# Kernel tuning notes

Hardware: AMD Instinct MI355X
Metric: run time of the kernel (lower is better)

## Reference

```python
import jax, jax.numpy as jnp
import numpy as np

B, C, H, W = 16, 128, 64, 64
L, ND = 512, 256
GROUPS = 32
EPS = 1e-6


def setup_inputs() -> dict:
    key = jax.random.key(0)
    ks = jax.random.split(key, 8)
    return {
        "x": jax.random.normal(ks[0], (B, C, H, W), dtype=jnp.float32),
        "nd": jax.random.normal(ks[1], (B, L, ND), dtype=jnp.float32),
        "gn_gamma": jnp.ones((C,), dtype=jnp.float32),
        "gn_beta": jnp.zeros((C,), dtype=jnp.float32),
        "q_w": jax.random.normal(ks[2], (C, C), dtype=jnp.float32) * 0.02,
        "q_b": jax.random.normal(ks[3], (C,), dtype=jnp.float32) * 0.02,
        "nd_w": jax.random.normal(ks[4], (C, ND), dtype=jnp.float32) * 0.02,
        "nd_b": jax.random.normal(ks[5], (C,), dtype=jnp.float32) * 0.02,
        "proj_w": jax.random.normal(ks[6], (C, C), dtype=jnp.float32) * 0.02,
        "proj_b": jax.random.normal(ks[7], (C,), dtype=jnp.float32) * 0.02,
    }


def _group_norm(x, gamma, beta):
    b, c, h, w = x.shape
    xr = x.reshape(b, GROUPS, c // GROUPS, h, w)
    mean = xr.mean(axis=(2, 3, 4), keepdims=True)
    var = xr.var(axis=(2, 3, 4), keepdims=True)
    xn = ((xr - mean) * jax.lax.rsqrt(var + EPS)).reshape(b, c, h, w)
    return xn * gamma[None, :, None, None] + beta[None, :, None, None]


def reference(x, nd, gn_gamma, gn_beta, q_w, q_b, nd_w, nd_b, proj_w, proj_b):
    b, c, h, w = x.shape
    hn = _group_norm(x, gn_gamma, gn_beta)
    # 1x1 conv query -> [b, hw, c]
    q = jnp.einsum('bchw,oc->bhwo', hn, q_w).reshape(b, h * w, c) + q_b
    # silu + linear projection of conditioning; k and v use identical projection/input
    kv = jax.nn.silu(nd) @ nd_w.T + nd_b  # [b, L, c]
    # attention: [b, hw, L]
    logits = jnp.einsum('bnc,blc->bnl', q, kv) * (c ** -0.5)
    attn = jax.nn.softmax(logits, axis=2)
    # weighted sum of v -> [b, c, hw] -> [b, c, h, w]
    out = jnp.einsum('blc,bnl->bcn', kv, attn).reshape(b, c, h, w)
    # 1x1 conv projection
    out = jnp.einsum('bchw,oc->bohw', out, proj_w) + proj_b[None, :, None, None]
    return x + out
```

## Files before the change

kernel.cpp:

```cpp
#include <hip/hip_runtime.h>
#include <math.h>

constexpr int kB = 16, kC = 128, kHW = 4096, kL = 512, kND = 256, kG = 32;
constexpr float kEps = 1e-6f;
constexpr float kScale = 0.08838834764831845f;

typedef short sv8 __attribute__((ext_vector_type(8)));
typedef int   iv4 __attribute__((ext_vector_type(4)));
typedef float f32x16 __attribute__((ext_vector_type(16)));

static __device__ __forceinline__ unsigned short f2bf(float f) {
    unsigned int u = __builtin_bit_cast(unsigned int, f);
    u += 0x7fffu + ((u >> 16) & 1u);
    return (unsigned short)(u >> 16);
}
static __device__ __forceinline__ float bf2f(unsigned short s) {
    unsigned int u = ((unsigned int)s) << 16;
    return __builtin_bit_cast(float, u);
}
static __device__ __forceinline__ unsigned int pack2(float a, float b) {
    return (unsigned int)f2bf(a) | ((unsigned int)f2bf(b) << 16);
}

#define GLOAD_LDS16(gp, lp)                                                     \
    __builtin_amdgcn_global_load_lds(                                           \
        (const __attribute__((address_space(1))) void*)(gp),                    \
        (__attribute__((address_space(3))) void*)(lp), 16, 0, 0)

__global__ __launch_bounds__(256) void prep_all_k(
    const float* __restrict__ x, const float* __restrict__ nd,
    const float* __restrict__ nd_w, const float* __restrict__ nd_b,
    const float* __restrict__ proj_w, const float* __restrict__ q_w,
    float* __restrict__ stats, unsigned short* __restrict__ kv_bf,
    unsigned short* __restrict__ kvT_bf, unsigned short* __restrict__ pwb,
    unsigned short* __restrict__ qwb)
{
    __shared__ float s_lds[8][256];
    __shared__ float w_lds[128][68];
    __shared__ float t_lds[8][129];
    __shared__ float red8[8];
    const int bid = blockIdx.x;
    const int tid = threadIdx.x;

    if (bid < 512) {
        const float4* p4 = (const float4*)(x + (size_t)bid * 4 * kHW);
        float s = 0.f, ss = 0.f;
        for (int i = tid; i < 4096; i += 256) {
            float4 v = p4[i];
            s  += (v.x + v.y) + (v.z + v.w);
            ss += (v.x * v.x + v.y * v.y) + (v.z * v.z + v.w * v.w);
        }
#pragma unroll
        for (int off = 1; off < 64; off <<= 1) {
            s  += __shfl_xor(s, off, 64);
            ss += __shfl_xor(ss, off, 64);
        }
        int wid = tid >> 6;
        if ((tid & 63) == 0) { red8[wid] = s; red8[wid + 4] = ss; }
        __syncthreads();
        if (tid == 0) {
            float S  = (red8[0] + red8[1]) + (red8[2] + red8[3]);
            float SS = (red8[4] + red8[5]) + (red8[6] + red8[7]);
            float mean = S * (1.f / 16384.f);
            float var  = SS * (1.f / 16384.f) - mean * mean;
            stats[bid * 2]     = mean;
            stats[bid * 2 + 1] = rsqrtf(var + kEps);
        }
        return;
    }
    if (bid >= 1536) {
        const float* src = (bid < 1552) ? proj_w : q_w;
        unsigned short* dst = (bid < 1552) ? pwb : qwb;
        int i = (((bid - 1536) & 15) * 256 + tid) * 4;
        float4 v = *(const float4*)(src + i);
        dst[i + 0] = f2bf(v.x); dst[i + 1] = f2bf(v.y);
        dst[i + 2] = f2bf(v.z); dst[i + 3] = f2bf(v.w);
        return;
    }
    {
        int idx0 = bid - 512;
        int b = idx0 >> 6;
        int l0 = (idx0 & 63) * 8;
        const float4* ndp = (const float4*)(nd + ((size_t)b * kL + l0) * kND);
#pragma unroll
        for (int r = 0; r < 2; r++) {
            int idx = tid + r * 256;
            int row = idx >> 6;
            int c4 = idx & 63;
            float4 v = ndp[row * 64 + c4];
            v.x = v.x / (1.f + __expf(-v.x));
            v.y = v.y / (1.f + __expf(-v.y));
            v.z = v.z / (1.f + __expf(-v.z));
            v.w = v.w / (1.f + __expf(-v.w));
            *(float4*)&s_lds[row][c4 * 4] = v;
        }
        float acc[4] = {0.f, 0.f, 0.f, 0.f};
        int lr = tid >> 5;
        int oq = tid & 31;
        for (int d0 = 0; d0 < kND; d0 += 64) {
            __syncthreads();
#pragma unroll
            for (int r = 0; r < 8; r++) {
                int idx = tid + r * 256;
                int row = idx >> 4;
                int c4 = idx & 15;
                float4 v = ((const float4*)(nd_w + (size_t)row * kND + d0))[c4];
                *(float4*)&w_lds[row][c4 * 4] = v;
            }
            __syncthreads();
            for (int dd = 0; dd < 64; dd += 4) {
                float4 sv = *(const float4*)&s_lds[lr][d0 + dd];
#pragma unroll
                for (int j = 0; j < 4; j++) {
                    float4 wv = *(const float4*)&w_lds[oq + 32 * j][dd];
                    acc[j] += sv.x * wv.x + sv.y * wv.y + sv.z * wv.z + sv.w * wv.w;
                }
            }
        }
#pragma unroll
        for (int j = 0; j < 4; j++) {
            int o = oq + 32 * j;
            float vout = acc[j] + nd_b[o];
            kv_bf[((size_t)b * kL + l0 + lr) * kC + o] = f2bf(vout);
            t_lds[lr][o] = vout;
        }
        __syncthreads();
        int o = tid >> 1, lh = (tid & 1) * 4;
        unsigned long long pk = 0;
#pragma unroll
        for (int i = 0; i < 4; i++)
            pk |= (unsigned long long)f2bf(t_lds[lh + i][o]) << (16 * i);
        *(unsigned long long*)(kvT_bf + ((size_t)b * kC + o) * kL + l0 + lh) = pk;
    }
}

__global__ __launch_bounds__(128, 2) void attn_k(
    const float* __restrict__ x,
    const float* __restrict__ stats,
    const float* __restrict__ gamma,
    const float* __restrict__ beta,
    const unsigned short* __restrict__ qwb,
    const float* __restrict__ q_b,
    const unsigned short* __restrict__ kvb,
    const unsigned short* __restrict__ kvtb,
    const unsigned short* __restrict__ pwb,
    const float* __restrict__ proj_b,
    float* __restrict__ out)
{
    __shared__ __align__(16) char smem[33024];

    const int flat = blockIdx.y * gridDim.x + blockIdx.x;
    const int b  = ((flat & 7) << 1) | ((flat >> 3) & 1);
    const int n0 = (flat >> 4) * 64;
    const int tid = threadIdx.x;
    const int wave = tid >> 6;
    const int lane = tid & 63;
    const int lrow = lane & 31;
    const int hi = lane >> 5;
    const int swzA = (lrow & 15) << 4;
    const int swzT = ((lrow >> 1) & 3) << 4;

    const unsigned short* kvB  = kvb  + (size_t)b * kL * kC;
    const unsigned short* kvtB = kvtb + (size_t)b * kC * kL;

#define STAGE_TILE(tt) do {                                                     \
        int l0s = (tt) << 5;                                                    \
        char* dA = smem + (((tt) & 1) * 8192);                                  \
        char* dT = smem + 16384 + (((tt) & 1) * 8192);                          \
        _Pragma("unroll")                                                       \
        for (int i = 0; i < 4; i++) {                                           \
            int idx = i * 128 + wave * 64 + lane;                               \
            int l = idx >> 4, ch = idx & 15;                                    \
            const unsigned short* gs =                                          \
                kvB + (size_t)(l0s + l) * kC + ((ch ^ (l & 15)) * 8);           \
            GLOAD_LDS16(gs, dA + (i * 128 + wave * 64) * 16);                   \
        }                                                                       \
        _Pragma("unroll")                                                       \
        for (int i = 0; i < 4; i++) {                                           \
            int idx = i * 128 + wave * 64 + lane;                               \
            int c = idx >> 2, ch = idx & 3;                                     \
            const unsigned short* gs =                                          \
                kvtB + (size_t)c * kL + l0s + ((ch ^ ((c >> 1) & 3)) * 8);      \
            GLOAD_LDS16(gs, dT + (i * 128 + wave * 64) * 16);                   \
        }                                                                       \
    } while (0)

    STAGE_TILE(0);

    float* hn_f = (float*)(smem + 8192);
    f32x16 dq[4];
#pragma unroll
    for (int ot = 0; ot < 4; ot++)
#pragma unroll
        for (int r = 0; r < 16; r++) dq[ot][r] = 0.f;

    for (int cc = 0; cc < 4; cc++) {
#pragma unroll
        for (int k = 0; k < 4; k++) {
            int cl = k * 8 + (tid >> 4);
            int c = cc * 32 + cl;
            int n4 = tid & 15;
            float4 v = *(const float4*)(
                x + ((size_t)b * kC + c) * kHW + n0 + n4 * 4);
            float mean = stats[(b * kG + (c >> 2)) * 2];
            float rstd = stats[(b * kG + (c >> 2)) * 2 + 1];
            float ga = gamma[c] * rstd;
            float be = beta[c] - mean * ga;
            v.x = v.x * ga + be; v.y = v.y * ga + be;
            v.z = v.z * ga + be; v.w = v.w * ga + be;
            *(float4*)&hn_f[cl * 64 + n4 * 4] = v;
        }
        __syncthreads();
        sv8 bh[2];
#pragma unroll
        for (int kk = 0; kk < 2; kk++) {
            sv8 a;
#pragma unroll
            for (int j = 0; j < 8; j++)
                a[j] = (short)f2bf(hn_f[(kk * 16 + hi * 8 + j) * 64 + wave * 32 + lrow]);
            bh[kk] = a;
        }
#pragma unroll
        for (int ot = 0; ot < 4; ot++) {
            const unsigned short* arow =
                qwb + (size_t)(ot * 32 + lrow) * kC + cc * 32 + hi * 8;
#pragma unroll
            for (int kk = 0; kk < 2; kk++)
                dq[ot] = __builtin_amdgcn_mfma_f32_32x32x16_bf16(
                             *(const sv8*)(arow + kk * 16), bh[kk], dq[ot], 0, 0, 0);
        }
        __syncthreads();
    }
    sv8 qa[8];
#pragma unroll
    for (int ot = 0; ot < 4; ot++) {
        unsigned int pk[4], pk2[4];
#pragma unroll
        for (int g = 0; g < 4; g++) {
            int ob = ot * 32 + 8 * g + 4 * hi;
            float4 qb4 = *(const float4*)(q_b + ob);
            float v0 = (dq[ot][4 * g + 0] + qb4.x) * kScale;
            float v1 = (dq[ot][4 * g + 1] + qb4.y) * kScale;
            float v2 = (dq[ot][4 * g + 2] + qb4.z) * kScale;
            float v3 = (dq[ot][4 * g + 3] + qb4.w) * kScale;
            pk[g]  = pack2(v0, v1);
            pk2[g] = pack2(v2, v3);
        }
#pragma unroll
        for (int kk = 0; kk < 2; kk++) {
            unsigned int a_lo = pk[kk * 2],  a_hi = pk[kk * 2 + 1];
            unsigned int b_lo = pk2[kk * 2], b_hi = pk2[kk * 2 + 1];
            unsigned int own_a = hi ? a_hi : a_lo;
            unsigned int own_b = hi ? b_hi : b_lo;
            unsigned int rcv_a = (unsigned int)__shfl_xor((int)(hi ? a_lo : a_hi), 32, 64);
            unsigned int rcv_b = (unsigned int)__shfl_xor((int)(hi ? b_lo : b_hi), 32, 64);
            iv4 w;
            w[0] = (int)(hi ? rcv_a : own_a);
            w[1] = (int)(hi ? rcv_b : own_b);
            w[2] = (int)(hi ? own_a : rcv_a);
            w[3] = (int)(hi ? own_b : rcv_b);
            qa[2 * ot + kk] = __builtin_bit_cast(sv8, w);
        }
    }

    f32x16 oacc[4];
#pragma unroll
    for (int ct = 0; ct < 4; ct++)
#pragma unroll
        for (int r = 0; r < 16; r++) oacc[ct][r] = 0.f;
    float rsumv = 0.f;

    for (int t = 0; t < 16; t++) {
        const char* bufA = smem + (t & 1) * 8192;
        const char* bufT = smem + 16384 + (t & 1) * 8192;
        if (t < 15) STAGE_TILE(t + 1);

        f32x16 s;
#pragma unroll
        for (int r = 0; r < 16; r++) s[r] = 0.f;
        {
            const char* arow = bufA + lrow * 256;
            __builtin_amdgcn_s_setprio(1);
#pragma unroll
            for (int kc = 0; kc < 8; kc++)
                s = __builtin_amdgcn_mfma_f32_32x32x16_bf16(
                        *(const sv8*)(arow + ((kc * 32 + hi * 16) ^ swzA)),
                        qa[kc], s, 0, 0, 0);
            __builtin_amdgcn_s_setprio(0);
        }
        float p[16];
#pragma unroll
        for (int r = 0; r < 16; r++) {
            p[r] = __expf(s[r]);
            rsumv += p[r];
        }
        unsigned int pk[4], pk2[4];
#pragma unroll
        for (int g = 0; g < 4; g++) {
            pk[g]  = pack2(p[4 * g + 0], p[4 * g + 1]);
            pk2[g] = pack2(p[4 * g + 2], p[4 * g + 3]);
        }
        sv8 pv[2];
#pragma unroll
        for (int kk = 0; kk < 2; kk++) {
            unsigned int a_lo = pk[kk * 2],  a_hi = pk[kk * 2 + 1];
            unsigned int b_lo = pk2[kk * 2], b_hi = pk2[kk * 2 + 1];
            unsigned int own_a = hi ? a_hi : a_lo;
            unsigned int own_b = hi ? b_hi : b_lo;
            unsigned int rcv_a = (unsigned int)__shfl_xor((int)(hi ? a_lo : a_hi), 32, 64);
            unsigned int rcv_b = (unsigned int)__shfl_xor((int)(hi ? b_lo : b_hi), 32, 64);
            iv4 w;
            w[0] = (int)(hi ? rcv_a : own_a);
            w[1] = (int)(hi ? rcv_b : own_b);
            w[2] = (int)(hi ? own_a : rcv_a);
            w[3] = (int)(hi ? own_b : rcv_b);
            pv[kk] = __builtin_bit_cast(sv8, w);
        }
        __builtin_amdgcn_s_setprio(1);
#pragma unroll
        for (int ct = 0; ct < 4; ct++) {
            const char* rowp = bufT + (ct * 32 + lrow) * 64;
#pragma unroll
            for (int kk = 0; kk < 2; kk++)
                oacc[ct] = __builtin_amdgcn_mfma_f32_32x32x16_bf16(
                               pv[kk],
                               *(const sv8*)(rowp + ((kk * 32 + hi * 16) ^ swzT)),
                               oacc[ct], 0, 0, 0);
        }
        __builtin_amdgcn_s_setprio(0);

        __syncthreads();
    }

    float total = rsumv + __shfl_xor(rsumv, 32, 64);
    float* rs = (float*)(smem + 32768) + wave * 32;
    rs[lrow] = 1.0f / total;
    float rinv[16];
#pragma unroll
    for (int r = 0; r < 16; r++)
        rinv[r] = rs[(r & 3) + 8 * (r >> 2) + 4 * hi];

    unsigned short* o_lds = (unsigned short*)smem;
    __syncthreads();
#pragma unroll
    for (int ct = 0; ct < 4; ct++)
#pragma unroll
        for (int r = 0; r < 16; r++) {
            int n = wave * 32 + (r & 3) + 8 * (r >> 2) + 4 * hi;
            o_lds[n * 136 + ct * 32 + lrow] = f2bf(oacc[ct][r] * rinv[r]);
        }
    sv8 oa[8];
    {
        const unsigned short* orow = o_lds + (wave * 32 + lrow) * 136 + hi * 8;
#pragma unroll
        for (int kc = 0; kc < 8; kc++) oa[kc] = *(const sv8*)(orow + kc * 16);
    }
    f32x16 dacc[4];
#pragma unroll
    for (int ot = 0; ot < 4; ot++)
#pragma unroll
        for (int r = 0; r < 16; r++) dacc[ot][r] = 0.f;
#pragma unroll
    for (int ot = 0; ot < 4; ot++) {
        const unsigned short* brow = pwb + (ot * 32 + lrow) * kC + hi * 8;
#pragma unroll
        for (int kc = 0; kc < 8; kc++)
            dacc[ot] = __builtin_amdgcn_mfma_f32_32x32x16_bf16(
                           oa[kc], *(const sv8*)(brow + kc * 16), dacc[ot], 0, 0, 0);
    }
#pragma unroll
    for (int ot = 0; ot < 4; ot++)
#pragma unroll
        for (int r = 0; r < 16; r++) {
            int n = wave * 32 + (r & 3) + 8 * (r >> 2) + 4 * hi;
            o_lds[n * 136 + ot * 32 + lrow] = f2bf(dacc[ot][r]);
        }
    __syncthreads();
#pragma unroll 4
    for (int it = 0; it < 64; it++) {
        int idx = it * 128 + tid;
        int o = idx >> 6, n = idx & 63;
        size_t gi = ((size_t)b * kC + o) * kHW + n0 + n;
        out[gi] = bf2f(o_lds[n * 136 + o]) + proj_b[o] + x[gi];
    }
#undef STAGE_TILE
}

extern "C" void kernel_launch(void* const* d_in, const int* in_sizes, int n_in,
                              void* d_out, int out_size, void* d_ws, size_t ws_size,
                              hipStream_t stream) {
    const float* x      = (const float*)d_in[0];
    const float* nd     = (const float*)d_in[1];
    const float* gamma  = (const float*)d_in[2];
    const float* beta   = (const float*)d_in[3];
    const float* q_w    = (const float*)d_in[4];
    const float* q_b    = (const float*)d_in[5];
    const float* nd_w   = (const float*)d_in[6];
    const float* nd_b   = (const float*)d_in[7];
    const float* proj_w = (const float*)d_in[8];
    const float* proj_b = (const float*)d_in[9];
    float* out = (float*)d_out;

    float* stats           = (float*)d_ws;
    unsigned short* pwb    = (unsigned short*)(stats + 1024);
    unsigned short* qwb    = pwb + 16384;
    unsigned short* kv_bf  = qwb + 16384;
    unsigned short* kvT_bf = kv_bf + (size_t)kB * kL * kC;

    prep_all_k<<<dim3(1568), dim3(256), 0, stream>>>(
        x, nd, nd_w, nd_b, proj_w, q_w, stats, kv_bf, kvT_bf, pwb, qwb);
    attn_k<<<dim3(kHW / 64, kB), dim3(128), 0, stream>>>(
        x, stats, gamma, beta, qwb, q_b, kv_bf, kvT_bf, pwb, proj_b, out);
}
```

Measured before the change: 87.84 us.

## Split query projection into separate kernel and widen attention blocks to four waves

Moves GroupNorm-apply plus the Q 1x1 projection out of the attention kernel into a new qproj_k kernel that writes bf16 Q to workspace. The attention kernel now loads Q directly and runs 256-thread blocks covering 128 positions, so each staged KV tile is shared by four waves instead of two. This halves KV staging traffic per position and shortens the attention kernel's prologue. In exchange it adds a kernel launch and a round trip of Q through global memory, and the larger blocks may lower occupancy.

```diff
diff --git a/kernel.cpp b/kernel.cpp
--- a/kernel.cpp
+++ b/kernel.cpp
@@ -134,72 +134,36 @@
     }
 }
 
-__global__ __launch_bounds__(128, 2) void attn_k(
-    const float* __restrict__ x,
-    const float* __restrict__ stats,
-    const float* __restrict__ gamma,
-    const float* __restrict__ beta,
-    const unsigned short* __restrict__ qwb,
-    const float* __restrict__ q_b,
-    const unsigned short* __restrict__ kvb,
-    const unsigned short* __restrict__ kvtb,
-    const unsigned short* __restrict__ pwb,
-    const float* __restrict__ proj_b,
-    float* __restrict__ out)
+__global__ __launch_bounds__(128, 4) void qproj_k(
+    const float* __restrict__ x, const float* __restrict__ stats,
+    const float* __restrict__ gamma, const float* __restrict__ beta,
+    const unsigned short* __restrict__ qwb, const float* __restrict__ q_b,
+    unsigned short* __restrict__ q_bf)
 {
-    __shared__ __align__(16) char smem[33024];
-
-    const int flat = blockIdx.y * gridDim.x + blockIdx.x;
-    const int b  = ((flat & 7) << 1) | ((flat >> 3) & 1);
-    const int n0 = (flat >> 4) * 64;
+    __shared__ __align__(16) char smem[8704];
+    float* hn_f = (float*)smem;
+    unsigned short* q_out = (unsigned short*)smem;
+
+    const int b = blockIdx.y;
+    const int n0 = blockIdx.x * 32;
     const int tid = threadIdx.x;
     const int wave = tid >> 6;
     const int lane = tid & 63;
     const int lrow = lane & 31;
     const int hi = lane >> 5;
-    const int swzA = (lrow & 15) << 4;
-    const int swzT = ((lrow >> 1) & 3) << 4;
-
-    const unsigned short* kvB  = kvb  + (size_t)b * kL * kC;
-    const unsigned short* kvtB = kvtb + (size_t)b * kC * kL;
-
-#define STAGE_TILE(tt) do {                                                     \
-        int l0s = (tt) << 5;                                                    \
-        char* dA = smem + (((tt) & 1) * 8192);                                  \
-        char* dT = smem + 16384 + (((tt) & 1) * 8192);                          \
-        _Pragma("unroll")                                                       \
-        for (int i = 0; i < 4; i++) {                                           \
-            int idx = i * 128 + wave * 64 + lane;                               \
-            int l = idx >> 4, ch = idx & 15;                                    \
-            const unsigned short* gs =                                          \
-                kvB + (size_t)(l0s + l) * kC + ((ch ^ (l & 15)) * 8);           \
-            GLOAD_LDS16(gs, dA + (i * 128 + wave * 64) * 16);                   \
-        }                                                                       \
-        _Pragma("unroll")                                                       \
-        for (int i = 0; i < 4; i++) {                                           \
-            int idx = i * 128 + wave * 64 + lane;                               \
-            int c = idx >> 2, ch = idx & 3;                                     \
-            const unsigned short* gs =                                          \
-                kvtB + (size_t)c * kL + l0s + ((ch ^ ((c >> 1) & 3)) * 8);      \
-            GLOAD_LDS16(gs, dT + (i * 128 + wave * 64) * 16);                   \
-        }                                                                       \
-    } while (0)
-
-    STAGE_TILE(0);
-
-    float* hn_f = (float*)(smem + 8192);
-    f32x16 dq[4];
-#pragma unroll
-    for (int ot = 0; ot < 4; ot++)
+
+    f32x16 dq[2];
+#pragma unroll
+    for (int ot = 0; ot < 2; ot++)
 #pragma unroll
         for (int r = 0; r < 16; r++) dq[ot][r] = 0.f;
 
     for (int cc = 0; cc < 4; cc++) {
 #pragma unroll
-        for (int k = 0; k < 4; k++) {
-            int cl = k * 8 + (tid >> 4);
+        for (int k = 0; k < 2; k++) {
+            int idx = tid + k * 128;
+            int cl = idx >> 3, n4 = idx & 7;
             int c = cc * 32 + cl;
-            int n4 = tid & 15;
             float4 v = *(const float4*)(
                 x + ((size_t)b * kC + c) * kHW + n0 + n4 * 4);
             float mean = stats[(b * kG + (c >> 2)) * 2];
@@ -208,7 +172,7 @@
             float be = beta[c] - mean * ga;
             v.x = v.x * ga + be; v.y = v.y * ga + be;
             v.z = v.z * ga + be; v.w = v.w * ga + be;
-            *(float4*)&hn_f[cl * 64 + n4 * 4] = v;
+            *(float4*)&hn_f[cl * 32 + n4 * 4] = v;
         }
         __syncthreads();
         sv8 bh[2];
@@ -217,13 +181,13 @@
             sv8 a;
 #pragma unroll
             for (int j = 0; j < 8; j++)
-                a[j] = (short)f2bf(hn_f[(kk * 16 + hi * 8 + j) * 64 + wave * 32 + lrow]);
+                a[j] = (short)f2bf(hn_f[(kk * 16 + hi * 8 + j) * 32 + lrow]);
             bh[kk] = a;
         }
 #pragma unroll
-        for (int ot = 0; ot < 4; ot++) {
+        for (int ot = 0; ot < 2; ot++) {
             const unsigned short* arow =
-                qwb + (size_t)(ot * 32 + lrow) * kC + cc * 32 + hi * 8;
+                qwb + (size_t)(wave * 64 + ot * 32 + lrow) * kC + cc * 32 + hi * 8;
 #pragma unroll
             for (int kk = 0; kk < 2; kk++)
                 dq[ot] = __builtin_amdgcn_mfma_f32_32x32x16_bf16(
@@ -231,36 +195,57 @@
         }
         __syncthreads();
     }
+#pragma unroll
+    for (int ot = 0; ot < 2; ot++) {
+#pragma unroll
+        for (int g = 0; g < 4; g++) {
+            int ob = wave * 64 + ot * 32 + 8 * g + 4 * hi;
+            float4 qb4 = *(const float4*)(q_b + ob);
+            q_out[lrow * 136 + ob + 0] = f2bf((dq[ot][4 * g + 0] + qb4.x) * kScale);
+            q_out[lrow * 136 + ob + 1] = f2bf((dq[ot][4 * g + 1] + qb4.y) * kScale);
+            q_out[lrow * 136 + ob + 2] = f2bf((dq[ot][4 * g + 2] + qb4.z) * kScale);
+            q_out[lrow * 136 + ob + 3] = f2bf((dq[ot][4 * g + 3] + qb4.w) * kScale);
+        }
+    }
+    __syncthreads();
+#pragma unroll
+    for (int r = 0; r < 4; r++) {
+        int idx = tid + r * 128;
+        int n = idx >> 4, ch = idx & 15;
+        *(uint4*)(q_bf + ((size_t)b * kHW + n0 + n) * kC + ch * 8) =
+            *(const uint4*)&q_out[n * 136 + ch * 8];
+    }
+}
+
+__global__ __launch_bounds__(256, 2) void attn_k(
+    const unsigned short* __restrict__ qb,
+    const unsigned short* __restrict__ kvb,
+    const unsigned short* __restrict__ kvtb,
+    const unsigned short* __restrict__ pwb,
+    const float* __restrict__ proj_b,
+    const float* __restrict__ x,
+    float* __restrict__ out)
+{
+    __shared__ __align__(16) char smem[35328];
+
+    const int flat = blockIdx.y * gridDim.x + blockIdx.x;
+    const int b  = ((flat & 7) << 1) | ((flat >> 3) & 1);
+    const int n0 = (flat >> 4) * 128;
+    const int tid = threadIdx.x;
+    const int wave = tid >> 6;
+    const int lane = tid & 63;
+    const int lrow = lane & 31;
+    const int hi = lane >> 5;
+    const int swzA = (lrow & 15) << 4;
+    const int swzT = ((lrow >> 1) & 3) << 4;
+
     sv8 qa[8];
-#pragma unroll
-    for (int ot = 0; ot < 4; ot++) {
-        unsigned int pk[4], pk2[4];
-#pragma unroll
-        for (int g = 0; g < 4; g++) {
-            int ob = ot * 32 + 8 * g + 4 * hi;
-            float4 qb4 = *(const float4*)(q_b + ob);
-            float v0 = (dq[ot][4 * g + 0] + qb4.x) * kScale;
-            float v1 = (dq[ot][4 * g + 1] + qb4.y) * kScale;
-            float v2 = (dq[ot][4 * g + 2] + qb4.z) * kScale;
-            float v3 = (dq[ot][4 * g + 3] + qb4.w) * kScale;
-            pk[g]  = pack2(v0, v1);
-            pk2[g] = pack2(v2, v3);
-        }
-#pragma unroll
-        for (int kk = 0; kk < 2; kk++) {
-            unsigned int a_lo = pk[kk * 2],  a_hi = pk[kk * 2 + 1];
-            unsigned int b_lo = pk2[kk * 2], b_hi = pk2[kk * 2 + 1];
-            unsigned int own_a = hi ? a_hi : a_lo;
-            unsigned int own_b = hi ? b_hi : b_lo;
-            unsigned int rcv_a = (unsigned int)__shfl_xor((int)(hi ? a_lo : a_hi), 32, 64);
-            unsigned int rcv_b = (unsigned int)__shfl_xor((int)(hi ? b_lo : b_hi), 32, 64);
-            iv4 w;
-            w[0] = (int)(hi ? rcv_a : own_a);
-            w[1] = (int)(hi ? rcv_b : own_b);
-            w[2] = (int)(hi ? own_a : rcv_a);
-            w[3] = (int)(hi ? own_b : rcv_b);
-            qa[2 * ot + kk] = __builtin_bit_cast(sv8, w);
-        }
+    {
+        const unsigned short* qrow =
+            qb + ((size_t)b * kHW + n0 + wave * 32 + lrow) * kC + hi * 8;
+#pragma unroll
+        for (int kc = 0; kc < 8; kc++)
+            qa[kc] = *(const sv8*)(qrow + kc * 16);
     }
 
     f32x16 oacc[4];
@@ -269,6 +254,34 @@
 #pragma unroll
         for (int r = 0; r < 16; r++) oacc[ct][r] = 0.f;
     float rsumv = 0.f;
+
+    const unsigned short* kvB  = kvb  + (size_t)b * kL * kC;
+    const unsigned short* kvtB = kvtb + (size_t)b * kC * kL;
+
+#define STAGE_TILE(tt) do {                                                     \
+        int l0s = (tt) << 5;                                                    \
+        char* dA = smem + (((tt) & 1) * 8192);                                  \
+        char* dT = smem + 16384 + (((tt) & 1) * 8192);                          \
+        _Pragma("unroll")                                                       \
+        for (int i = 0; i < 2; i++) {                                           \
+            int l = i * 16 + wave * 4 + (lane >> 4);                            \
+            int ch = lane & 15;                                                 \
+            const unsigned short* gs =                                          \
+                kvB + (size_t)(l0s + l) * kC + ((ch ^ (l & 15)) * 8);           \
+            GLOAD_LDS16(gs, dA + (i * 256 + wave * 64) * 16);                   \
+        }                                                                       \
+        _Pragma("unroll")                                                       \
+        for (int i = 0; i < 2; i++) {                                           \
+            int c = i * 64 + wave * 16 + (lane >> 2);                           \
+            int ch = lane & 3;                                                  \
+            const unsigned short* gs =                                          \
+                kvtB + (size_t)c * kL + l0s + ((ch ^ ((c >> 1) & 3)) * 8);      \
+            GLOAD_LDS16(gs, dT + (i * 256 + wave * 64) * 16);                   \
+        }                                                                       \
+    } while (0)
+
+    STAGE_TILE(0);
+    __syncthreads();
 
     for (int t = 0; t < 16; t++) {
         const char* bufA = smem + (t & 1) * 8192;
@@ -333,7 +346,7 @@
     }
 
     float total = rsumv + __shfl_xor(rsumv, 32, 64);
-    float* rs = (float*)(smem + 32768) + wave * 32;
+    float* rs = (float*)(smem + 34816) + wave * 32;
     rs[lrow] = 1.0f / total;
     float rinv[16];
 #pragma unroll
@@ -378,8 +391,8 @@
     __syncthreads();
 #pragma unroll 4
     for (int it = 0; it < 64; it++) {
-        int idx = it * 128 + tid;
-        int o = idx >> 6, n = idx & 63;
+        int idx = it * 256 + tid;
+        int o = idx >> 7, n = idx & 127;
         size_t gi = ((size_t)b * kC + o) * kHW + n0 + n;
         out[gi] = bf2f(o_lds[n * 136 + o]) + proj_b[o] + x[gi];
     }
@@ -406,9 +419,12 @@
     unsigned short* qwb    = pwb + 16384;
     unsigned short* kv_bf  = qwb + 16384;
     unsigned short* kvT_bf = kv_bf + (size_t)kB * kL * kC;
+    unsigned short* q_bf   = kvT_bf + (size_t)kB * kL * kC;
 
     prep_all_k<<<dim3(1568), dim3(256), 0, stream>>>(
         x, nd, nd_w, nd_b, proj_w, q_w, stats, kv_bf, kvT_bf, pwb, qwb);
-    attn_k<<<dim3(kHW / 64, kB), dim3(128), 0, stream>>>(
-        x, stats, gamma, beta, qwb, q_b, kv_bf, kvT_bf, pwb, proj_b, out);
-}
+    qproj_k<<<dim3(kHW / 32, kB), dim3(128), 0, stream>>>(
+        x, stats, gamma, beta, qwb, q_b, q_bf);
+    attn_k<<<dim3(kHW / 128, kB), dim3(256), 0, stream>>>(
+        q_bf, kv_bf, kvT_bf, pwb, proj_b, x, out);
+}
```

Result: slower. 93.99 us (+7.0%).

## Double attention tile to 128 pixels with 4 waves sharing KV tiles

Applied to the files above, without the earlier changes.

The attention kernel now processes 128 spatial positions per block using 256 threads (four waves), so each staged K/V tile in LDS is shared by twice as many query rows. This halves the number of blocks that reload the same KV data and the per-block staging overhead. The group-norm scale and shift are also folded into per-channel gamma/beta coefficients in the prep kernel and cached in LDS with q_b. The cost is more LDS per block (51 KB), which may lower occupancy.

```diff
diff --git a/kernel.cpp b/kernel.cpp
--- a/kernel.cpp
+++ b/kernel.cpp
@@ -31,7 +31,8 @@
     const float* __restrict__ x, const float* __restrict__ nd,
     const float* __restrict__ nd_w, const float* __restrict__ nd_b,
     const float* __restrict__ proj_w, const float* __restrict__ q_w,
-    float* __restrict__ stats, unsigned short* __restrict__ kv_bf,
+    const float* __restrict__ gamma, const float* __restrict__ beta,
+    float* __restrict__ gab, unsigned short* __restrict__ kv_bf,
     unsigned short* __restrict__ kvT_bf, unsigned short* __restrict__ pwb,
     unsigned short* __restrict__ qwb)
 {
@@ -63,8 +64,16 @@
             float SS = (red8[4] + red8[5]) + (red8[6] + red8[7]);
             float mean = S * (1.f / 16384.f);
             float var  = SS * (1.f / 16384.f) - mean * mean;
-            stats[bid * 2]     = mean;
-            stats[bid * 2 + 1] = rsqrtf(var + kEps);
+            red8[0] = mean;
+            red8[1] = rsqrtf(var + kEps);
+        }
+        __syncthreads();
+        if (tid < 4) {
+            int bb = bid >> 5, g = bid & 31, c = g * 4 + tid;
+            float mean = red8[0], rstd = red8[1];
+            float ga = gamma[c] * rstd;
+            gab[bb * 256 + c]       = ga;
+            gab[bb * 256 + 128 + c] = beta[c] - mean * ga;
         }
         return;
     }
@@ -134,24 +143,22 @@
     }
 }
 
-__global__ __launch_bounds__(128, 2) void attn_k(
+__global__ __launch_bounds__(256, 2) void attn_k(
     const float* __restrict__ x,
-    const float* __restrict__ stats,
-    const float* __restrict__ gamma,
-    const float* __restrict__ beta,
+    const float* __restrict__ gab,
+    const float* __restrict__ q_b,
     const unsigned short* __restrict__ qwb,
-    const float* __restrict__ q_b,
     const unsigned short* __restrict__ kvb,
     const unsigned short* __restrict__ kvtb,
     const unsigned short* __restrict__ pwb,
     const float* __restrict__ proj_b,
     float* __restrict__ out)
 {
-    __shared__ __align__(16) char smem[33024];
+    __shared__ __align__(16) char smem[51200];
 
     const int flat = blockIdx.y * gridDim.x + blockIdx.x;
     const int b  = ((flat & 7) << 1) | ((flat >> 3) & 1);
-    const int n0 = (flat >> 4) * 64;
+    const int n0 = (flat >> 4) * 128;
     const int tid = threadIdx.x;
     const int wave = tid >> 6;
     const int lane = tid & 63;
@@ -160,6 +167,9 @@
     const int swzA = (lrow & 15) << 4;
     const int swzT = ((lrow >> 1) & 3) << 4;
 
+    float* x_lds = (float*)(smem + 32768);
+    float* gtab  = (float*)(smem + 49152);
+
     const unsigned short* kvB  = kvb  + (size_t)b * kL * kC;
     const unsigned short* kvtB = kvtb + (size_t)b * kC * kL;
 
@@ -168,26 +178,31 @@
         char* dA = smem + (((tt) & 1) * 8192);                                  \
         char* dT = smem + 16384 + (((tt) & 1) * 8192);                          \
         _Pragma("unroll")                                                       \
-        for (int i = 0; i < 4; i++) {                                           \
-            int idx = i * 128 + wave * 64 + lane;                               \
-            int l = idx >> 4, ch = idx & 15;                                    \
+        for (int i = 0; i < 2; i++) {                                           \
+            int l = i * 16 + wave * 4 + (lane >> 4);                            \
+            int ch = lane & 15;                                                 \
             const unsigned short* gs =                                          \
                 kvB + (size_t)(l0s + l) * kC + ((ch ^ (l & 15)) * 8);           \
-            GLOAD_LDS16(gs, dA + (i * 128 + wave * 64) * 16);                   \
+            GLOAD_LDS16(gs, dA + (i * 256 + wave * 64) * 16);                   \
         }                                                                       \
         _Pragma("unroll")                                                       \
-        for (int i = 0; i < 4; i++) {                                           \
-            int idx = i * 128 + wave * 64 + lane;                               \
-            int c = idx >> 2, ch = idx & 3;                                     \
+        for (int i = 0; i < 2; i++) {                                           \
+            int c = i * 64 + wave * 16 + (lane >> 2);                           \
+            int ch = lane & 3;                                                  \
             const unsigned short* gs =                                          \
                 kvtB + (size_t)c * kL + l0s + ((ch ^ ((c >> 1) & 3)) * 8);      \
-            GLOAD_LDS16(gs, dT + (i * 128 + wave * 64) * 16);                   \
+            GLOAD_LDS16(gs, dT + (i * 256 + wave * 64) * 16);                   \
         }                                                                       \
     } while (0)
 
     STAGE_TILE(0);
 
-    float* hn_f = (float*)(smem + 8192);
+    if (tid < 64)
+        ((float4*)gtab)[tid] = ((const float4*)(gab + b * 256))[tid];
+    else if (tid < 96)
+        ((float4*)gtab)[tid] = ((const float4*)q_b)[tid - 64];
+    __syncthreads();
+
     f32x16 dq[4];
 #pragma unroll
     for (int ot = 0; ot < 4; ot++)
@@ -197,40 +212,34 @@
     for (int cc = 0; cc < 4; cc++) {
 #pragma unroll
         for (int k = 0; k < 4; k++) {
-            int cl = k * 8 + (tid >> 4);
-            int c = cc * 32 + cl;
-            int n4 = tid & 15;
+            int idx = tid + k * 256;
+            int c = idx >> 5, n4 = idx & 31;
+            int cg = cc * 32 + c;
             float4 v = *(const float4*)(
-                x + ((size_t)b * kC + c) * kHW + n0 + n4 * 4);
-            float mean = stats[(b * kG + (c >> 2)) * 2];
-            float rstd = stats[(b * kG + (c >> 2)) * 2 + 1];
-            float ga = gamma[c] * rstd;
-            float be = beta[c] - mean * ga;
+                x + ((size_t)b * kC + cg) * kHW + n0 + n4 * 4);
+            float ga = gtab[cg], be = gtab[128 + cg];
             v.x = v.x * ga + be; v.y = v.y * ga + be;
             v.z = v.z * ga + be; v.w = v.w * ga + be;
-            *(float4*)&hn_f[cl * 64 + n4 * 4] = v;
-        }
-        __syncthreads();
-        sv8 bh[2];
+            *(float4*)&x_lds[c * 128 + n4 * 4] = v;
+        }
+        __syncthreads();
 #pragma unroll
         for (int kk = 0; kk < 2; kk++) {
-            sv8 a;
+            sv8 bh;
 #pragma unroll
             for (int j = 0; j < 8; j++)
-                a[j] = (short)f2bf(hn_f[(kk * 16 + hi * 8 + j) * 64 + wave * 32 + lrow]);
-            bh[kk] = a;
-        }
-#pragma unroll
-        for (int ot = 0; ot < 4; ot++) {
-            const unsigned short* arow =
-                qwb + (size_t)(ot * 32 + lrow) * kC + cc * 32 + hi * 8;
-#pragma unroll
-            for (int kk = 0; kk < 2; kk++)
+                bh[j] = (short)f2bf(x_lds[(kk * 16 + hi * 8 + j) * 128 + wave * 32 + lrow]);
+#pragma unroll
+            for (int ot = 0; ot < 4; ot++) {
+                const unsigned short* arow =
+                    qwb + (size_t)(ot * 32 + lrow) * kC + cc * 32 + kk * 16 + hi * 8;
                 dq[ot] = __builtin_amdgcn_mfma_f32_32x32x16_bf16(
-                             *(const sv8*)(arow + kk * 16), bh[kk], dq[ot], 0, 0, 0);
-        }
-        __syncthreads();
-    }
+                             *(const sv8*)arow, bh, dq[ot], 0, 0, 0);
+            }
+        }
+        __syncthreads();
+    }
+
     sv8 qa[8];
 #pragma unroll
     for (int ot = 0; ot < 4; ot++) {
@@ -238,7 +247,7 @@
 #pragma unroll
         for (int g = 0; g < 4; g++) {
             int ob = ot * 32 + 8 * g + 4 * hi;
-            float4 qb4 = *(const float4*)(q_b + ob);
+            float4 qb4 = *(const float4*)&gtab[256 + ob];
             float v0 = (dq[ot][4 * g + 0] + qb4.x) * kScale;
             float v1 = (dq[ot][4 * g + 1] + qb4.y) * kScale;
             float v2 = (dq[ot][4 * g + 2] + qb4.z) * kScale;
@@ -333,7 +342,7 @@
     }
 
     float total = rsumv + __shfl_xor(rsumv, 32, 64);
-    float* rs = (float*)(smem + 32768) + wave * 32;
+    float* rs = (float*)(smem + 50688) + wave * 32;
     rs[lrow] = 1.0f / total;
     float rinv[16];
 #pragma unroll
@@ -378,8 +387,8 @@
     __syncthreads();
 #pragma unroll 4
     for (int it = 0; it < 64; it++) {
-        int idx = it * 128 + tid;
-        int o = idx >> 6, n = idx & 63;
+        int idx = it * 256 + tid;
+        int o = idx >> 7, n = idx & 127;
         size_t gi = ((size_t)b * kC + o) * kHW + n0 + n;
         out[gi] = bf2f(o_lds[n * 136 + o]) + proj_b[o] + x[gi];
     }
@@ -401,14 +410,14 @@
     const float* proj_b = (const float*)d_in[9];
     float* out = (float*)d_out;
 
-    float* stats           = (float*)d_ws;
-    unsigned short* pwb    = (unsigned short*)(stats + 1024);
+    float* gab             = (float*)d_ws;
+    unsigned short* pwb    = (unsigned short*)(gab + 4096);
     unsigned short* qwb    = pwb + 16384;
     unsigned short* kv_bf  = qwb + 16384;
     unsigned short* kvT_bf = kv_bf + (size_t)kB * kL * kC;
 
     prep_all_k<<<dim3(1568), dim3(256), 0, stream>>>(
-        x, nd, nd_w, nd_b, proj_w, q_w, stats, kv_bf, kvT_bf, pwb, qwb);
-    attn_k<<<dim3(kHW / 64, kB), dim3(128), 0, stream>>>(
-        x, stats, gamma, beta, qwb, q_b, kv_bf, kvT_bf, pwb, proj_b, out);
-}
+        x, nd, nd_w, nd_b, proj_w, q_w, gamma, beta, gab, kv_bf, kvT_bf, pwb, qwb);
+    attn_k<<<dim3(kHW / 128, kB), dim3(256), 0, stream>>>(
+        x, gab, q_b, qwb, kv_bf, kvT_bf, pwb, proj_b, out);
+}
```

Measured after the change: 82.13 us. 6.5% less time.
